# Kernel tuning notes

Measured on AMD Instinct MI355X. Metric: run time of the kernel, lower is better.

Reference implementation:

```python
import jax, jax.numpy as jnp
import numpy as np

B, N, L, E, D = 16, 16384, 192, 128, 128


def setup_inputs() -> dict:
    key = jax.random.key(0)
    ks = jax.random.split(key, 16)
    s = 0.05
    return {
        "x_L_flattened": jax.random.normal(ks[0], (B, N), jnp.float32),
        "x_y_mask_flattened": jax.random.randint(ks[1], (B, N), 0, 2).astype(jnp.float32),
        "y_mask_L_flattened": jnp.zeros((B, N), jnp.float32),
        "x_y_mark": jax.random.normal(ks[2], (B, L, 1), jnp.float32),
        "variable_indices_flattened": jax.random.randint(ks[3], (B, N), 0, E),
        "time_indices_flattened": jax.random.randint(ks[4], (B, N), 0, L),
        "N_OBSERVATIONS_MAX": N,
        # learned params (stored [in, out]; torch Linear uses x @ W.T + b)
        "W_obs": jax.random.normal(ks[5], (2, D), jnp.float32) * s,
        "b_obs": jnp.zeros((D,), jnp.float32),
        "W_time": jax.random.normal(ks[6], (1, D), jnp.float32) * s,
        "b_time": jnp.zeros((D,), jnp.float32),
        "var_hyperedge_w": jax.random.normal(ks[7], (E, D), jnp.float32),
        "W_q": jax.random.normal(ks[8], (D, D), jnp.float32) * s,
        "b_q": jnp.zeros((D,), jnp.float32),
        "W_k": jax.random.normal(ks[9], (D, D), jnp.float32) * s,
        "b_k": jnp.zeros((D,), jnp.float32),
        "W_v": jax.random.normal(ks[10], (D, D), jnp.float32) * s,
        "b_v": jnp.zeros((D,), jnp.float32),
        "threshold": jnp.float32(0.5),
        "merge_coef": jnp.float32(0.5),
    }


def reference(x_L_flattened, x_y_mask_flattened, y_mask_L_flattened, x_y_mark,
              variable_indices_flattened, time_indices_flattened, N_OBSERVATIONS_MAX,
              W_obs, b_obs, W_time, b_time, var_hyperedge_w,
              W_q, b_q, W_k, b_k, W_v, b_v, threshold, merge_coef):
    mask = x_y_mask_flattened  # [B, N]
    # node features: value + (1 - mask + y_mask) channel -> [B, N, 2]
    feats = jnp.stack([x_L_flattened, 1.0 - mask + y_mask_L_flattened], axis=-1)
    # temporal incidence: node n belongs to time-edge l iff time_idx[n] == l; [B, L, N]
    ti = (time_indices_flattened[:, None, :] == jnp.arange(L)[None, :, None]).astype(jnp.float32)
    ti = ti * mask[:, None, :]
    # variable incidence: node n belongs to var-edge e iff var_idx[n] == e; [B, E, N]
    vi = (jnp.arange(E)[None, :, None] == variable_indices_flattened[:, None, :]).astype(jnp.float32)
    vi = vi * mask[:, None, :]
    # encoders
    obs = jax.nn.relu(feats @ W_obs + b_obs) * mask[..., None]          # [B, N, D]
    temp_he = jnp.sin(x_y_mark @ W_time + b_time)                        # [B, L, D]
    var_he = jax.nn.relu(jnp.broadcast_to(var_hyperedge_w, (B, E, D)))   # [B, E, D]
    # IrregularityAwareAttention over variable hyperedges with incidence as aux
    q = var_he @ W_q + b_q
    k = var_he @ W_k + b_k
    v = var_he @ W_v + b_v
    att = jnp.einsum('bed,bfd->bef', q, k) / (D ** 0.5)                  # [B, E, E]
    att_aux = jnp.einsum('ben,bfn->bef', vi, vi) / (N_OBSERVATIONS_MAX ** 0.5)
    merge = (att > threshold) & (att_aux != 0)
    att = jnp.where(merge, (1.0 - merge_coef) * att + merge_coef * att_aux, att)
    attn = jax.nn.softmax(att, axis=-1)
    out = jnp.einsum('bef,bfd->bed', attn, v)                            # [B, E, D]
    return (obs, temp_he, out, ti, vi)
```

## Files before the change

kernel.cpp:

```cpp
#include <hip/hip_runtime.h>

#define Bb 16
#define Nn 16384
#define Ll 192
#define Ee 128
#define Dd 128


__global__ __launch_bounds__(256) void k_inc(
    const int* __restrict__ tidx, const int* __restrict__ vidx,
    const float* __restrict__ mask,
    float* __restrict__ ti, float* __restrict__ vi, float* __restrict__ cnt)
{
    __shared__ float hcnt[Ee];
    const int tid = threadIdx.x;
    if (tid < Ee) hcnt[tid] = 0.0f;
    __syncthreads();

    const int g  = blockIdx.x * 256 + tid;
    const int b  = g >> 12;
    const int n4 = (g & 4095) << 2;

    const int4   t4 = *reinterpret_cast<const int4*>(tidx + b * Nn + n4);
    const int4   v4 = *reinterpret_cast<const int4*>(vidx + b * Nn + n4);
    const float4 m4 = *reinterpret_cast<const float4*>(mask + b * Nn + n4);

    if (m4.x != 0.0f) atomicAdd(&hcnt[v4.x], 1.0f);
    if (m4.y != 0.0f) atomicAdd(&hcnt[v4.y], 1.0f);
    if (m4.z != 0.0f) atomicAdd(&hcnt[v4.z], 1.0f);
    if (m4.w != 0.0f) atomicAdd(&hcnt[v4.w], 1.0f);

    float* tib = ti + (((size_t)b * Ll) << 14) + n4;
    #pragma unroll 4
    for (int l = 0; l < Ll; ++l) {
        float4 o;
        o.x = (t4.x == l) ? m4.x : 0.0f;
        o.y = (t4.y == l) ? m4.y : 0.0f;
        o.z = (t4.z == l) ? m4.z : 0.0f;
        o.w = (t4.w == l) ? m4.w : 0.0f;
        *reinterpret_cast<float4*>(tib + ((size_t)l << 14)) = o;
    }

    float* vib = vi + (((size_t)b * Ee) << 14) + n4;
    #pragma unroll 4
    for (int e = 0; e < Ee; ++e) {
        float4 o;
        o.x = (v4.x == e) ? m4.x : 0.0f;
        o.y = (v4.y == e) ? m4.y : 0.0f;
        o.z = (v4.z == e) ? m4.z : 0.0f;
        o.w = (v4.w == e) ? m4.w : 0.0f;
        *reinterpret_cast<float4*>(vib + ((size_t)e << 14)) = o;
    }

    __syncthreads();
    if (tid < Ee) {
        const float c = hcnt[tid];
        if (c != 0.0f) atomicAdd(&cnt[b * Ee + tid], c);
    }
}

__global__ __launch_bounds__(256) void k_obs(
    const float* __restrict__ x, const float* __restrict__ mask,
    const float* __restrict__ ymask, const float* __restrict__ W_obs,
    const float* __restrict__ b_obs, float* __restrict__ obs)
{
    const int g   = blockIdx.x * 256 + threadIdx.x;
    const int row = g >> 5;
    const int d   = (g & 31) << 2;

    const float m  = mask[row];
    const float xv = x[row];
    const float f1 = 1.0f - m + ymask[row];

    const float4 w0 = *reinterpret_cast<const float4*>(W_obs + d);
    const float4 w1 = *reinterpret_cast<const float4*>(W_obs + Dd + d);
    const float4 bb = *reinterpret_cast<const float4*>(b_obs + d);

    float4 o;
    o.x = fmaxf(fmaf(xv, w0.x, fmaf(f1, w1.x, bb.x)), 0.0f) * m;
    o.y = fmaxf(fmaf(xv, w0.y, fmaf(f1, w1.y, bb.y)), 0.0f) * m;
    o.z = fmaxf(fmaf(xv, w0.z, fmaf(f1, w1.z, bb.z)), 0.0f) * m;
    o.w = fmaxf(fmaf(xv, w0.w, fmaf(f1, w1.w, bb.w)), 0.0f) * m;
    *reinterpret_cast<float4*>(obs + ((size_t)row << 7) + d) = o;
}

__global__ __launch_bounds__(256) void k_temp(
    const float* __restrict__ mark, const float* __restrict__ Wt,
    const float* __restrict__ bt, float* __restrict__ temp)
{
    const int idx = blockIdx.x * 256 + threadIdx.x;
    const int d = idx & 127;
    const int r = idx >> 7;
    temp[idx] = sinf(fmaf(mark[r], Wt[d], bt[d]));
}

__global__ __launch_bounds__(128) void k_qkv(
    const float* __restrict__ var_w,
    const float* __restrict__ Wq, const float* __restrict__ bq,
    const float* __restrict__ Wk, const float* __restrict__ bk,
    const float* __restrict__ Wv, const float* __restrict__ bv,
    float* __restrict__ q, float* __restrict__ k, float* __restrict__ v)
{
    __shared__ float h[Dd];
    const int e = blockIdx.x, d = threadIdx.x;
    h[d] = fmaxf(var_w[e * Dd + d], 0.0f);
    __syncthreads();
    float aq = bq[d], ak = bk[d], av = bv[d];
    #pragma unroll 4
    for (int j = 0; j < Dd; ++j) {
        const float hj = h[j];
        aq = fmaf(hj, Wq[j * Dd + d], aq);
        ak = fmaf(hj, Wk[j * Dd + d], ak);
        av = fmaf(hj, Wv[j * Dd + d], av);
    }
    q[e * Dd + d] = aq;
    k[e * Dd + d] = ak;
    v[e * Dd + d] = av;
}

__global__ __launch_bounds__(128) void k_att0(
    const float* __restrict__ q, const float* __restrict__ k,
    float* __restrict__ att0)
{
    __shared__ float qr[Dd];
    const int e = blockIdx.x, f = threadIdx.x;
    qr[f] = q[e * Dd + f];
    __syncthreads();
    const float* kr = k + f * Dd;
    float acc = 0.0f;
    #pragma unroll 4
    for (int d = 0; d < Dd; ++d) acc = fmaf(qr[d], kr[d], acc);
    att0[e * Dd + f] = acc * 0.08838834764831845f;
}

__global__ __launch_bounds__(128) void k_soft(
    const float* __restrict__ att0, const float* __restrict__ v,
    const float* __restrict__ cnt, const float* __restrict__ thr_p,
    const float* __restrict__ mc_p, const int* __restrict__ nobs_p,
    float* __restrict__ outp)
{
    __shared__ float attn[Ee];
    __shared__ float red[4];
    const int b = blockIdx.x >> 7;
    const int e = blockIdx.x & 127;
    const int f = threadIdx.x;

    float a = att0[e * Ee + f];
    if (f == e) {
        const float c = cnt[b * Ee + e];
        const float thr = *thr_p;
        if (c != 0.0f && a > thr) {
            const float mc  = *mc_p;
            const float aux = c / sqrtf((float)(*nobs_p));
            a = (1.0f - mc) * a + mc * aux;
        }
    }
    float mx = a;
    #pragma unroll
    for (int off = 32; off > 0; off >>= 1) mx = fmaxf(mx, __shfl_xor(mx, off));
    if ((threadIdx.x & 63) == 0) red[threadIdx.x >> 6] = mx;
    __syncthreads();
    mx = fmaxf(red[0], red[1]);

    const float ex = expf(a - mx);
    float s = ex;
    #pragma unroll
    for (int off = 32; off > 0; off >>= 1) s += __shfl_xor(s, off);
    if ((threadIdx.x & 63) == 0) red[2 + (threadIdx.x >> 6)] = s;
    __syncthreads();
    s = red[2] + red[3];

    attn[f] = ex / s;
    __syncthreads();

    const int d = f;
    float acc = 0.0f;
    #pragma unroll 4
    for (int j = 0; j < Ee; ++j) acc = fmaf(attn[j], v[j * Dd + d], acc);
    outp[((size_t)(b * Ee + e) << 7) + d] = acc;
}

extern "C" void kernel_launch(void* const* d_in, const int* in_sizes, int n_in,
                              void* d_out, int out_size, void* d_ws, size_t ws_size,
                              hipStream_t stream) {
    (void)in_sizes; (void)n_in; (void)out_size; (void)ws_size;

    const float* x      = (const float*)d_in[0];
    const float* mask   = (const float*)d_in[1];
    const float* ymask  = (const float*)d_in[2];
    const float* mark   = (const float*)d_in[3];
    const int*   vidx   = (const int*)d_in[4];
    const int*   tidx   = (const int*)d_in[5];
    const int*   nobs   = (const int*)d_in[6];
    const float* W_obs  = (const float*)d_in[7];
    const float* b_obs  = (const float*)d_in[8];
    const float* W_time = (const float*)d_in[9];
    const float* b_time = (const float*)d_in[10];
    const float* var_w  = (const float*)d_in[11];
    const float* W_q    = (const float*)d_in[12];
    const float* b_q    = (const float*)d_in[13];
    const float* W_k    = (const float*)d_in[14];
    const float* b_k    = (const float*)d_in[15];
    const float* W_v    = (const float*)d_in[16];
    const float* b_v    = (const float*)d_in[17];
    const float* thr    = (const float*)d_in[18];
    const float* mc     = (const float*)d_in[19];

    float* out_base = (float*)d_out;
    float* obs  = out_base;
    float* temp = out_base + 33554432;
    float* attO = out_base + 33947648;
    float* ti   = out_base + 34209792;
    float* vi   = out_base + 84541440;

    float* ws   = (float*)d_ws;
    float* cnt  = ws;
    float* q    = ws + 2048;
    float* k    = ws + 18432;
    float* v    = ws + 34816;
    float* att0 = ws + 51200;

    hipMemsetAsync(cnt, 0, 2048 * sizeof(float), stream);

    k_inc<<<(Bb * Nn) / (4 * 256), 256, 0, stream>>>(tidx, vidx, mask, ti, vi, cnt);
    k_obs<<<(Bb * Nn * 32) / 256, 256, 0, stream>>>(x, mask, ymask, W_obs, b_obs, obs);
    k_temp<<<(Bb * Ll * Dd) / 256, 256, 0, stream>>>(mark, W_time, b_time, temp);
    k_qkv<<<Ee, Dd, 0, stream>>>(var_w, W_q, b_q, W_k, b_k, W_v, b_v, q, k, v);
    k_att0<<<Ee, Dd, 0, stream>>>(q, k, att0);
    k_soft<<<Bb * Ee, Dd, 0, stream>>>(att0, v, cnt, thr, mc, nobs, attO);
}
```

Before: 591.0 us.

## Merge kernels into three launches and split incidence writes across more blocks

```diff
diff --git a/kernel.cpp b/kernel.cpp
--- a/kernel.cpp
+++ b/kernel.cpp
@@ -7,147 +7,150 @@
 #define Dd 128
 
 
-__global__ __launch_bounds__(256) void k_inc(
+__global__ __launch_bounds__(256) void k_front(
     const int* __restrict__ tidx, const int* __restrict__ vidx,
-    const float* __restrict__ mask,
-    float* __restrict__ ti, float* __restrict__ vi, float* __restrict__ cnt)
-{
-    __shared__ float hcnt[Ee];
-    const int tid = threadIdx.x;
-    if (tid < Ee) hcnt[tid] = 0.0f;
-    __syncthreads();
-
-    const int g  = blockIdx.x * 256 + tid;
-    const int b  = g >> 12;
-    const int n4 = (g & 4095) << 2;
-
-    const int4   t4 = *reinterpret_cast<const int4*>(tidx + b * Nn + n4);
-    const int4   v4 = *reinterpret_cast<const int4*>(vidx + b * Nn + n4);
-    const float4 m4 = *reinterpret_cast<const float4*>(mask + b * Nn + n4);
-
-    if (m4.x != 0.0f) atomicAdd(&hcnt[v4.x], 1.0f);
-    if (m4.y != 0.0f) atomicAdd(&hcnt[v4.y], 1.0f);
-    if (m4.z != 0.0f) atomicAdd(&hcnt[v4.z], 1.0f);
-    if (m4.w != 0.0f) atomicAdd(&hcnt[v4.w], 1.0f);
-
-    float* tib = ti + (((size_t)b * Ll) << 14) + n4;
-    #pragma unroll 4
-    for (int l = 0; l < Ll; ++l) {
-        float4 o;
-        o.x = (t4.x == l) ? m4.x : 0.0f;
-        o.y = (t4.y == l) ? m4.y : 0.0f;
-        o.z = (t4.z == l) ? m4.z : 0.0f;
-        o.w = (t4.w == l) ? m4.w : 0.0f;
-        *reinterpret_cast<float4*>(tib + ((size_t)l << 14)) = o;
-    }
-
-    float* vib = vi + (((size_t)b * Ee) << 14) + n4;
-    #pragma unroll 4
-    for (int e = 0; e < Ee; ++e) {
-        float4 o;
-        o.x = (v4.x == e) ? m4.x : 0.0f;
-        o.y = (v4.y == e) ? m4.y : 0.0f;
-        o.z = (v4.z == e) ? m4.z : 0.0f;
-        o.w = (v4.w == e) ? m4.w : 0.0f;
-        *reinterpret_cast<float4*>(vib + ((size_t)e << 14)) = o;
-    }
-
-    __syncthreads();
-    if (tid < Ee) {
-        const float c = hcnt[tid];
-        if (c != 0.0f) atomicAdd(&cnt[b * Ee + tid], c);
-    }
-}
-
-__global__ __launch_bounds__(256) void k_obs(
-    const float* __restrict__ x, const float* __restrict__ mask,
-    const float* __restrict__ ymask, const float* __restrict__ W_obs,
-    const float* __restrict__ b_obs, float* __restrict__ obs)
-{
-    const int g   = blockIdx.x * 256 + threadIdx.x;
-    const int row = g >> 5;
-    const int d   = (g & 31) << 2;
-
-    const float m  = mask[row];
-    const float xv = x[row];
-    const float f1 = 1.0f - m + ymask[row];
-
-    const float4 w0 = *reinterpret_cast<const float4*>(W_obs + d);
-    const float4 w1 = *reinterpret_cast<const float4*>(W_obs + Dd + d);
-    const float4 bb = *reinterpret_cast<const float4*>(b_obs + d);
-
-    float4 o;
-    o.x = fmaxf(fmaf(xv, w0.x, fmaf(f1, w1.x, bb.x)), 0.0f) * m;
-    o.y = fmaxf(fmaf(xv, w0.y, fmaf(f1, w1.y, bb.y)), 0.0f) * m;
-    o.z = fmaxf(fmaf(xv, w0.z, fmaf(f1, w1.z, bb.z)), 0.0f) * m;
-    o.w = fmaxf(fmaf(xv, w0.w, fmaf(f1, w1.w, bb.w)), 0.0f) * m;
-    *reinterpret_cast<float4*>(obs + ((size_t)row << 7) + d) = o;
-}
-
-__global__ __launch_bounds__(256) void k_temp(
-    const float* __restrict__ mark, const float* __restrict__ Wt,
-    const float* __restrict__ bt, float* __restrict__ temp)
-{
-    const int idx = blockIdx.x * 256 + threadIdx.x;
-    const int d = idx & 127;
-    const int r = idx >> 7;
-    temp[idx] = sinf(fmaf(mark[r], Wt[d], bt[d]));
-}
-
-__global__ __launch_bounds__(128) void k_qkv(
-    const float* __restrict__ var_w,
+    const float* __restrict__ mask, const float* __restrict__ var_w,
     const float* __restrict__ Wq, const float* __restrict__ bq,
     const float* __restrict__ Wk, const float* __restrict__ bk,
     const float* __restrict__ Wv, const float* __restrict__ bv,
-    float* __restrict__ q, float* __restrict__ k, float* __restrict__ v)
+    float* __restrict__ ti, float* __restrict__ vi,
+    float* __restrict__ cnt_part,
+    float* __restrict__ q, float* __restrict__ kT, float* __restrict__ v)
 {
-    __shared__ float h[Dd];
-    const int e = blockIdx.x, d = threadIdx.x;
-    h[d] = fmaxf(var_w[e * Dd + d], 0.0f);
-    __syncthreads();
-    float aq = bq[d], ak = bk[d], av = bv[d];
-    #pragma unroll 4
-    for (int j = 0; j < Dd; ++j) {
-        const float hj = h[j];
-        aq = fmaf(hj, Wq[j * Dd + d], aq);
-        ak = fmaf(hj, Wk[j * Dd + d], ak);
-        av = fmaf(hj, Wv[j * Dd + d], av);
+    __shared__ float sh[Ee];
+    const int tid = threadIdx.x;
+
+    if (blockIdx.x < 1024) {
+        const int pb      = blockIdx.x >> 2;
+        const int quarter = blockIdx.x & 3;
+        const int g  = pb * 256 + tid;
+        const int b  = g >> 12;
+        const int n4 = (g & 4095) << 2;
+
+        const int4   t4 = *reinterpret_cast<const int4*>(tidx + b * Nn + n4);
+        const int4   v4 = *reinterpret_cast<const int4*>(vidx + b * Nn + n4);
+        const float4 m4 = *reinterpret_cast<const float4*>(mask + b * Nn + n4);
+
+        if (quarter == 0) {
+            if (tid < Ee) sh[tid] = 0.0f;
+            __syncthreads();
+            if (m4.x != 0.0f) atomicAdd(&sh[v4.x], 1.0f);
+            if (m4.y != 0.0f) atomicAdd(&sh[v4.y], 1.0f);
+            if (m4.z != 0.0f) atomicAdd(&sh[v4.z], 1.0f);
+            if (m4.w != 0.0f) atomicAdd(&sh[v4.w], 1.0f);
+        }
+
+        const int l0 = quarter * 48;
+        float* tib = ti + (((size_t)b * Ll) << 14) + n4;
+        #pragma unroll 4
+        for (int l = l0; l < l0 + 48; ++l) {
+            float4 o;
+            o.x = (t4.x == l) ? m4.x : 0.0f;
+            o.y = (t4.y == l) ? m4.y : 0.0f;
+            o.z = (t4.z == l) ? m4.z : 0.0f;
+            o.w = (t4.w == l) ? m4.w : 0.0f;
+            *reinterpret_cast<float4*>(tib + ((size_t)l << 14)) = o;
+        }
+
+        const int e0 = quarter * 32;
+        float* vib = vi + (((size_t)b * Ee) << 14) + n4;
+        #pragma unroll 4
+        for (int e = e0; e < e0 + 32; ++e) {
+            float4 o;
+            o.x = (v4.x == e) ? m4.x : 0.0f;
+            o.y = (v4.y == e) ? m4.y : 0.0f;
+            o.z = (v4.z == e) ? m4.z : 0.0f;
+            o.w = (v4.w == e) ? m4.w : 0.0f;
+            *reinterpret_cast<float4*>(vib + ((size_t)e << 14)) = o;
+        }
+
+        if (quarter == 0) {
+            __syncthreads();
+            if (tid < Ee) cnt_part[pb * Ee + tid] = sh[tid];
+        }
+    } else {
+        const int e = blockIdx.x - 1024;
+        const int d = tid;
+        if (d < Dd) sh[d] = fmaxf(var_w[e * Dd + d], 0.0f);
+        __syncthreads();
+        if (d < Dd) {
+            float aq = bq[d], ak = bk[d], av = bv[d];
+            #pragma unroll 4
+            for (int j = 0; j < Dd; ++j) {
+                const float hj = sh[j];
+                aq = fmaf(hj, Wq[j * Dd + d], aq);
+                ak = fmaf(hj, Wk[j * Dd + d], ak);
+                av = fmaf(hj, Wv[j * Dd + d], av);
+            }
+            q[e * Dd + d]  = aq;
+            kT[d * Dd + e] = ak;
+            v[e * Dd + d]  = av;
+        }
     }
-    q[e * Dd + d] = aq;
-    k[e * Dd + d] = ak;
-    v[e * Dd + d] = av;
-}
-
-__global__ __launch_bounds__(128) void k_att0(
-    const float* __restrict__ q, const float* __restrict__ k,
-    float* __restrict__ att0)
+}
+
+__global__ __launch_bounds__(256) void k_back(
+    const float* __restrict__ x, const float* __restrict__ mask,
+    const float* __restrict__ ymask, const float* __restrict__ W_obs,
+    const float* __restrict__ b_obs, const float* __restrict__ mark,
+    const float* __restrict__ Wt, const float* __restrict__ bt,
+    float* __restrict__ obs, float* __restrict__ temp)
+{
+    if (blockIdx.x < 32768) {
+        const int g   = blockIdx.x * 256 + threadIdx.x;
+        const int row = g >> 5;
+        const int d   = (g & 31) << 2;
+
+        const float m  = mask[row];
+        const float xv = x[row];
+        const float f1 = 1.0f - m + ymask[row];
+
+        const float4 w0 = *reinterpret_cast<const float4*>(W_obs + d);
+        const float4 w1 = *reinterpret_cast<const float4*>(W_obs + Dd + d);
+        const float4 bb = *reinterpret_cast<const float4*>(b_obs + d);
+
+        float4 o;
+        o.x = fmaxf(fmaf(xv, w0.x, fmaf(f1, w1.x, bb.x)), 0.0f) * m;
+        o.y = fmaxf(fmaf(xv, w0.y, fmaf(f1, w1.y, bb.y)), 0.0f) * m;
+        o.z = fmaxf(fmaf(xv, w0.z, fmaf(f1, w1.z, bb.z)), 0.0f) * m;
+        o.w = fmaxf(fmaf(xv, w0.w, fmaf(f1, w1.w, bb.w)), 0.0f) * m;
+        *reinterpret_cast<float4*>(obs + ((size_t)row << 7) + d) = o;
+    } else {
+        const int idx = (blockIdx.x - 32768) * 256 + threadIdx.x;
+        const int d = idx & 127;
+        const int r = idx >> 7;
+        temp[idx] = sinf(fmaf(mark[r], Wt[d], bt[d]));
+    }
+}
+
+__global__ __launch_bounds__(128) void k_soft(
+    const float* __restrict__ q, const float* __restrict__ kT,
+    const float* __restrict__ v, const float* __restrict__ cnt_part,
+    const float* __restrict__ thr_p, const float* __restrict__ mc_p,
+    const int* __restrict__ nobs_p, float* __restrict__ outp)
 {
     __shared__ float qr[Dd];
-    const int e = blockIdx.x, f = threadIdx.x;
-    qr[f] = q[e * Dd + f];
-    __syncthreads();
-    const float* kr = k + f * Dd;
-    float acc = 0.0f;
-    #pragma unroll 4
-    for (int d = 0; d < Dd; ++d) acc = fmaf(qr[d], kr[d], acc);
-    att0[e * Dd + f] = acc * 0.08838834764831845f;
-}
-
-__global__ __launch_bounds__(128) void k_soft(
-    const float* __restrict__ att0, const float* __restrict__ v,
-    const float* __restrict__ cnt, const float* __restrict__ thr_p,
-    const float* __restrict__ mc_p, const int* __restrict__ nobs_p,
-    float* __restrict__ outp)
-{
     __shared__ float attn[Ee];
-    __shared__ float red[4];
+    __shared__ float red[5];
     const int b = blockIdx.x >> 7;
     const int e = blockIdx.x & 127;
     const int f = threadIdx.x;
 
-    float a = att0[e * Ee + f];
+    qr[f] = q[e * Dd + f];
+
+    float cp = (f < 16) ? cnt_part[(b * 16 + f) * Ee + e] : 0.0f;
+    #pragma unroll
+    for (int off = 8; off > 0; off >>= 1) cp += __shfl_xor(cp, off);
+    if (f == 0) red[4] = cp;
+    __syncthreads();
+
+    float acc0 = 0.0f;
+    #pragma unroll 4
+    for (int d = 0; d < Dd; ++d) acc0 = fmaf(qr[d], kT[d * Dd + f], acc0);
+    float a = acc0 * 0.08838834764831845f;
+
     if (f == e) {
-        const float c = cnt[b * Ee + e];
+        const float c = red[4];
         const float thr = *thr_p;
         if (c != 0.0f && a > thr) {
             const float mc  = *mc_p;
@@ -155,10 +158,11 @@
             a = (1.0f - mc) * a + mc * aux;
         }
     }
+
     float mx = a;
     #pragma unroll
     for (int off = 32; off > 0; off >>= 1) mx = fmaxf(mx, __shfl_xor(mx, off));
-    if ((threadIdx.x & 63) == 0) red[threadIdx.x >> 6] = mx;
+    if ((f & 63) == 0) red[f >> 6] = mx;
     __syncthreads();
     mx = fmaxf(red[0], red[1]);
 
@@ -166,7 +170,7 @@
     float s = ex;
     #pragma unroll
     for (int off = 32; off > 0; off >>= 1) s += __shfl_xor(s, off);
-    if ((threadIdx.x & 63) == 0) red[2 + (threadIdx.x >> 6)] = s;
+    if ((f & 63) == 0) red[2 + (f >> 6)] = s;
     __syncthreads();
     s = red[2] + red[3];
 
@@ -213,19 +217,16 @@
     float* ti   = out_base + 34209792;
     float* vi   = out_base + 84541440;
 
-    float* ws   = (float*)d_ws;
-    float* cnt  = ws;
-    float* q    = ws + 2048;
-    float* k    = ws + 18432;
-    float* v    = ws + 34816;
-    float* att0 = ws + 51200;
-
-    hipMemsetAsync(cnt, 0, 2048 * sizeof(float), stream);
-
-    k_inc<<<(Bb * Nn) / (4 * 256), 256, 0, stream>>>(tidx, vidx, mask, ti, vi, cnt);
-    k_obs<<<(Bb * Nn * 32) / 256, 256, 0, stream>>>(x, mask, ymask, W_obs, b_obs, obs);
-    k_temp<<<(Bb * Ll * Dd) / 256, 256, 0, stream>>>(mark, W_time, b_time, temp);
-    k_qkv<<<Ee, Dd, 0, stream>>>(var_w, W_q, b_q, W_k, b_k, W_v, b_v, q, k, v);
-    k_att0<<<Ee, Dd, 0, stream>>>(q, k, att0);
-    k_soft<<<Bb * Ee, Dd, 0, stream>>>(att0, v, cnt, thr, mc, nobs, attO);
-}
+    float* ws       = (float*)d_ws;
+    float* cnt_part = ws;
+    float* q        = ws + 32768;
+    float* kT       = ws + 49152;
+    float* v        = ws + 65536;
+
+    k_front<<<1024 + 128, 256, 0, stream>>>(tidx, vidx, mask, var_w,
+                                            W_q, b_q, W_k, b_k, W_v, b_v,
+                                            ti, vi, cnt_part, q, kT, v);
+    k_back<<<32768 + 1536, 256, 0, stream>>>(x, mask, ymask, W_obs, b_obs,
+                                             mark, W_time, b_time, obs, temp);
+    k_soft<<<Bb * Ee, Dd, 0, stream>>>(q, kT, v, cnt_part, thr, mc, nobs, attO);
+}
```

Result: no change. 583.2 us (-1.3%).
